# Performance work log

Measured on AMD Instinct MI355X. Metric: run time of the kernel, lower is better.

## Reference

```python
import jax, jax.numpy as jnp
import numpy as np

B, S, D, H = 4, 2048, 1024, 16
HD = D // H


def setup_inputs() -> dict:
    key = jax.random.key(0)
    ks = jax.random.split(key, 12)
    scale = 1.0 / np.sqrt(D)
    inp = {
        "query": jax.random.normal(ks[0], (B, S, D), jnp.float32),
        "key": jax.random.normal(ks[1], (B, S, D), jnp.float32),
        "value": jax.random.normal(ks[2], (B, S, D), jnp.float32),
        "mask": jax.random.randint(ks[3], (B, 1, S, S), 0, 2).astype(jnp.float32),
        "Wq": jax.random.normal(ks[4], (D, D), jnp.float32) * scale,
        "bq": jnp.zeros((D,), jnp.float32),
        "Wk": jax.random.normal(ks[5], (D, D), jnp.float32) * scale,
        "bk": jnp.zeros((D,), jnp.float32),
        "Wv": jax.random.normal(ks[6], (D, D), jnp.float32) * scale,
        "bv": jnp.zeros((D,), jnp.float32),
        "Wo": jax.random.normal(ks[7], (D, D), jnp.float32) * scale,
        "bo": jnp.zeros((D,), jnp.float32),
    }
    return inp


def reference(query, key, value, mask, Wq, bq, Wk, bk, Wv, bv, Wo, bo):
    # projections, then split heads: [B, S, D] -> [B, H, S, HD]
    def split_heads(x):
        return x.reshape(B, S, H, HD).transpose(0, 2, 1, 3)

    q = split_heads(query @ Wq + bq)
    k = split_heads(key @ Wk + bk)
    v = split_heads(value @ Wv + bv)

    # scores [B, H, Sq, Sk]
    logits = jnp.einsum("bhqd,bhkd->bhqk", q, k) / jnp.sqrt(jnp.float32(HD))
    logits = logits + mask * (-1e9)
    attn = jax.nn.softmax(logits, axis=-1)
    out = jnp.einsum("bhqk,bhkd->bhqd", attn, v)  # [B, H, Sq, HD]
    out = out.transpose(0, 2, 1, 3).reshape(B, S, D)
    return out @ Wo + bo
```

## Files before the change

kernel.cpp:

```cpp
#include <hip/hip_runtime.h>

#define DI __device__ __forceinline__

typedef __attribute__((ext_vector_type(8))) short short8v;
typedef __attribute__((ext_vector_type(4))) float f32x4;

static constexpr int B_ = 4, S_ = 2048, D_ = 1024, H_ = 16, HD_ = 64;
static constexpr int M_ = B_ * S_;

DI unsigned short f2bf(float f) {
  unsigned u = __builtin_bit_cast(unsigned, f);
  u = (u + 0x7fffu + ((u >> 16) & 1u)) >> 16;
  return (unsigned short)u;
}

DI unsigned cvt_pk_bf16(float lo, float hi) {
  unsigned r;
  asm("v_cvt_pk_bf16_f32 %0, %1, %2" : "=v"(r) : "v"(lo), "v"(hi));
  return r;
}

DI void async_copy16(const void* g, void* l) {
  __builtin_amdgcn_global_load_lds((const __attribute__((address_space(1))) void*)g,
                                   (__attribute__((address_space(3))) void*)l, 16, 0, 0);
}

__global__ __launch_bounds__(256) void cast_bf16_kernel(const float* __restrict__ in,
                                                        unsigned short* __restrict__ out,
                                                        int n4) {
  int i = blockIdx.x * blockDim.x + threadIdx.x;
  int stride = gridDim.x * blockDim.x;
  for (; i < n4; i += stride) {
    float4 v = reinterpret_cast<const float4*>(in)[i];
    ushort4 o;
    o.x = f2bf(v.x); o.y = f2bf(v.y); o.z = f2bf(v.z); o.w = f2bf(v.w);
    reinterpret_cast<ushort4*>(out)[i] = o;
  }
}

__global__ __launch_bounds__(256) void transpose_cast_kernel(const float* __restrict__ W,
                                                             unsigned short* __restrict__ Wt,
                                                             int n) {
  __shared__ float t[32][33];
  int bx = blockIdx.x * 32, by = blockIdx.y * 32;
  int x = threadIdx.x, y0 = threadIdx.y;
#pragma unroll
  for (int yy = 0; yy < 32; yy += 8)
    t[y0 + yy][x] = W[(long)(by + y0 + yy) * n + bx + x];
  __syncthreads();
#pragma unroll
  for (int yy = 0; yy < 32; yy += 8)
    Wt[(long)(bx + y0 + yy) * n + by + x] = f2bf(t[x][y0 + yy]);
}

__global__ __launch_bounds__(256) void pack_mask_kernel(const float* __restrict__ mask,
                                                        unsigned long long* __restrict__ bits,
                                                        int nwords) {
  int lane = threadIdx.x & 63;
  int wpb = blockDim.x >> 6;
  int w = blockIdx.x * wpb + (threadIdx.x >> 6);
  int stride = gridDim.x * wpb;
  for (; w < nwords; w += stride) {
    float v = mask[(long)w * 64 + lane];
    unsigned long long b = __ballot(v > 0.5f);
    if (lane == 0) {
      int bb = w >> 16, q = (w >> 5) & 2047, kt64 = w & 31;
      bits[((long)bb << 16) | (kt64 << 11) | q] = b;
    }
  }
}

template <int MODE>
__global__ __launch_bounds__(256) void gemm_bt_kernel(const unsigned short* __restrict__ A,
                                                      const unsigned short* __restrict__ Bt,
                                                      const float* __restrict__ bias,
                                                      void* __restrict__ out,
                                                      int Mdim, int Ndim, int Kdim, float scale) {
  __shared__ unsigned short As[3][128 * 32];
  __shared__ unsigned short Bs[3][128 * 32];
  const int tid = threadIdx.x;
  const int lane = tid & 63;
  const int w = tid >> 6;
  const int g = lane >> 4;
  const int l15 = lane & 15;
  const int bm = blockIdx.x * 128;
  const int bn = blockIdx.y * 128;
  const int wr = w >> 1, wc = w & 1;

  f32x4 zero = {0.f, 0.f, 0.f, 0.f};
  f32x4 acc[4][4];
#pragma unroll
  for (int i = 0; i < 4; ++i)
#pragma unroll
    for (int j = 0; j < 4; ++j) acc[i][j] = zero;

  const int srow = lane >> 2;
  const int scol = (lane & 3) * 8;

  auto stageg = [&](int k0, int bi) {
#pragma unroll
    for (int i = 0; i < 2; ++i) {
      int q = w * 2 + i;
      int row = q * 16 + srow;
      async_copy16(&A[(long)(bm + row) * Kdim + k0 + scol], &As[bi][q * 512]);
      async_copy16(&Bt[(long)(bn + row) * Kdim + k0 + scol], &Bs[bi][q * 512]);
    }
  };

  const int NT = Kdim / 32;
  stageg(0, 0);
  stageg(32, 1);
  asm volatile("s_waitcnt vmcnt(4)" ::: "memory");
  __builtin_amdgcn_sched_barrier(0);
  __builtin_amdgcn_s_barrier();
  asm volatile("" ::: "memory");

  for (int t = 0; t < NT; ++t) {
    if (t + 2 < NT) stageg((t + 2) * 32, (t + 2) % 3);

    const unsigned short* Ab = &As[t % 3][0];
    const unsigned short* Bb = &Bs[t % 3][0];
    short8v a[4], b[4];
#pragma unroll
    for (int i = 0; i < 4; ++i)
      a[i] = *reinterpret_cast<const short8v*>(&Ab[(wr * 64 + i * 16 + l15) * 32 + g * 8]);
#pragma unroll
    for (int j = 0; j < 4; ++j)
      b[j] = *reinterpret_cast<const short8v*>(&Bb[(wc * 64 + j * 16 + l15) * 32 + g * 8]);
#pragma unroll
    for (int i = 0; i < 4; ++i)
#pragma unroll
      for (int j = 0; j < 4; ++j)
        acc[i][j] = __builtin_amdgcn_mfma_f32_16x16x32_bf16(a[i], b[j], acc[i][j], 0, 0, 0);

    if (t + 2 < NT) {
      asm volatile("s_waitcnt vmcnt(4) lgkmcnt(0)" ::: "memory");
    } else {
      asm volatile("s_waitcnt vmcnt(0) lgkmcnt(0)" ::: "memory");
    }
    __builtin_amdgcn_sched_barrier(0);
    __builtin_amdgcn_s_barrier();
    asm volatile("" ::: "memory");
  }

#pragma unroll
  for (int jj = 0; jj < 4; ++jj) {
    int n = bn + wc * 64 + jj * 16 + l15;
    float bs = bias[n];
#pragma unroll
    for (int i = 0; i < 4; ++i) {
      int m0 = bm + wr * 64 + i * 16 + g * 4;
      if (MODE == 0) {
        unsigned short* o = (unsigned short*)out;
#pragma unroll
        for (int r = 0; r < 4; ++r)
          o[(long)(m0 + r) * Ndim + n] = f2bf((acc[i][jj][r] + bs) * scale);
      } else if (MODE == 1) {
        int b2 = m0 >> 11, s0 = m0 & 2047;
        int s0p = (s0 & ~31) | (((s0 >> 2) & 3) << 3) | (((s0 >> 4) & 1) << 2);
        int h2 = n >> 6, d2 = n & 63;
        unsigned short* o = (unsigned short*)out;
        ushort4 v;
        v.x = f2bf(acc[i][jj][0] + bs);
        v.y = f2bf(acc[i][jj][1] + bs);
        v.z = f2bf(acc[i][jj][2] + bs);
        v.w = f2bf(acc[i][jj][3] + bs);
        *reinterpret_cast<ushort4*>(&o[((long)((b2 * 16 + h2) * 64 + d2) << 11) + s0p]) = v;
      } else {
        float* o = (float*)out;
#pragma unroll
        for (int r = 0; r < 4; ++r)
          o[(long)(m0 + r) * Ndim + n] = acc[i][jj][r] + bs;
      }
    }
  }
}

__global__ __launch_bounds__(256, 4) void attn_kernel(const unsigned short* __restrict__ Q,
                                                      const unsigned short* __restrict__ Kb,
                                                      const unsigned short* __restrict__ Vt,
                                                      const unsigned long long* __restrict__ mbits,
                                                      unsigned short* __restrict__ attn) {
  __shared__ unsigned short Ks[2][64 * 64];
  __shared__ unsigned short Vs[2][64 * 64];
  const int lane = threadIdx.x & 63;
  const int w = threadIdx.x >> 6;
  const int g = lane >> 4;
  const int l15 = lane & 15;
  const int qt = blockIdx.x;
  const int bh = blockIdx.y;
  const int b = bh >> 4, h = bh & 15;
  const int q0 = qt * 64 + w * 16 + l15;

  const unsigned short* qp = Q + ((long)b * S_ + q0) * D_ + h * HD_ + g * 8;
  short8v qf0 = *reinterpret_cast<const short8v*>(qp);
  short8v qf1 = *reinterpret_cast<const short8v*>(qp + 32);

  const int srow = lane >> 3;
  const int schunk = ((lane & 7) ^ (lane >> 3)) * 8;
  const unsigned short* kstage = Kb + (long)b * S_ * D_ + h * HD_;
  const unsigned short* vstage = Vt + (long)bh * HD_ * S_;

  f32x4 zero = {0.f, 0.f, 0.f, 0.f};
  f32x4 oacc[4] = {zero, zero, zero, zero};
  float m_run = -1e30f, l_run = 0.f;

  const unsigned long long* mbase = mbits + ((long)b << 16);
  const int swz = l15 & 7;

  auto stage = [&](int kt, int bi) {
#pragma unroll
    for (int i = 0; i < 2; ++i) {
      int blk8 = w * 2 + i;
      async_copy16(&kstage[(long)(kt + blk8 * 8 + srow) * D_ + schunk], &Ks[bi][blk8 * 512]);
      async_copy16(&vstage[(long)(blk8 * 8 + srow) * S_ + kt + schunk], &Vs[bi][blk8 * 512]);
    }
  };

  unsigned long long mw_cur = mbase[q0];
  stage(0, 0);

  int cur = 0;
  for (int t = 0; t < S_ / 64; ++t) {
    unsigned long long mw_nxt = 0;
    if (t < S_ / 64 - 1) {
      mw_nxt = mbase[((t + 1) << 11) + q0];
      stage((t + 1) * 64, cur ^ 1);
      asm volatile("s_waitcnt vmcnt(5)" ::: "memory");
    } else {
      asm volatile("s_waitcnt vmcnt(0)" ::: "memory");
    }
    __builtin_amdgcn_s_barrier();
    asm volatile("" ::: "memory");

    const unsigned short* Kbuf = &Ks[cur][0];
    const unsigned short* Vbuf = &Vs[cur][0];

    f32x4 lt[4];
    __builtin_amdgcn_s_setprio(1);
#pragma unroll
    for (int g2 = 0; g2 < 4; ++g2) {
      const unsigned short* kr = &Kbuf[(g2 * 16 + l15) * 64];
      short8v kf0 = *reinterpret_cast<const short8v*>(&kr[(g ^ swz) * 8]);
      short8v kf1 = *reinterpret_cast<const short8v*>(&kr[((g + 4) ^ swz) * 8]);
      f32x4 c = zero;
      c = __builtin_amdgcn_mfma_f32_16x16x32_bf16(kf0, qf0, c, 0, 0, 0);
      c = __builtin_amdgcn_mfma_f32_16x16x32_bf16(kf1, qf1, c, 0, 0, 0);
      lt[g2] = c;
    }
    __builtin_amdgcn_s_setprio(0);

    float tmax = -1e30f;
#pragma unroll
    for (int g2 = 0; g2 < 4; ++g2)
#pragma unroll
      for (int r = 0; r < 4; ++r) {
        int krel = g2 * 16 + g * 4 + r;
        float v = ((mw_cur >> krel) & 1ull) ? -1e30f : lt[g2][r];
        lt[g2][r] = v;
        tmax = fmaxf(tmax, v);
      }
    tmax = fmaxf(tmax, __shfl_xor(tmax, 16));
    tmax = fmaxf(tmax, __shfl_xor(tmax, 32));
    float m_new = fmaxf(m_run, tmax);
    float alpha = __builtin_amdgcn_exp2f(m_run - m_new);
    float p[4][4];
    float tsum = 0.f;
#pragma unroll
    for (int g2 = 0; g2 < 4; ++g2)
#pragma unroll
      for (int r = 0; r < 4; ++r) {
        p[g2][r] = __builtin_amdgcn_exp2f(lt[g2][r] - m_new);
        tsum += p[g2][r];
      }
    tsum += __shfl_xor(tsum, 16);
    tsum += __shfl_xor(tsum, 32);
    l_run = l_run * alpha + tsum;
    m_run = m_new;
#pragma unroll
    for (int d = 0; d < 4; ++d) oacc[d] *= alpha;
    short8v pfr[2];
#pragma unroll
    for (int s = 0; s < 2; ++s) {
      union { unsigned u[4]; short8v v; } pu;
      pu.u[0] = cvt_pk_bf16(p[2 * s][0], p[2 * s][1]);
      pu.u[1] = cvt_pk_bf16(p[2 * s][2], p[2 * s][3]);
      pu.u[2] = cvt_pk_bf16(p[2 * s + 1][0], p[2 * s + 1][1]);
      pu.u[3] = cvt_pk_bf16(p[2 * s + 1][2], p[2 * s + 1][3]);
      pfr[s] = pu.v;
    }

    __builtin_amdgcn_s_setprio(1);
#pragma unroll
    for (int d0 = 0; d0 < 4; ++d0) {
      const unsigned short* vr = &Vbuf[(d0 * 16 + l15) * 64];
#pragma unroll
      for (int s = 0; s < 2; ++s) {
        short8v vf = *reinterpret_cast<const short8v*>(&vr[((s * 4 + g) ^ swz) * 8]);
        oacc[d0] = __builtin_amdgcn_mfma_f32_16x16x32_bf16(vf, pfr[s], oacc[d0], 0, 0, 0);
      }
    }
    __builtin_amdgcn_s_setprio(0);

    asm volatile("" ::: "memory");
    __builtin_amdgcn_s_barrier();
    asm volatile("" ::: "memory");
    mw_cur = mw_nxt;
    cur ^= 1;
  }

  float inv = 1.f / l_run;
#pragma unroll
  for (int d0 = 0; d0 < 4; ++d0) {
    ushort4 o;
    o.x = f2bf(oacc[d0][0] * inv);
    o.y = f2bf(oacc[d0][1] * inv);
    o.z = f2bf(oacc[d0][2] * inv);
    o.w = f2bf(oacc[d0][3] * inv);
    *reinterpret_cast<ushort4*>(&attn[((long)b * S_ + q0) * D_ + h * HD_ + d0 * 16 + g * 4]) = o;
  }
}

extern "C" void kernel_launch(void* const* d_in, const int* in_sizes, int n_in,
                              void* d_out, int out_size, void* d_ws, size_t ws_size,
                              hipStream_t stream) {
  const float* query = (const float*)d_in[0];
  const float* key   = (const float*)d_in[1];
  const float* value = (const float*)d_in[2];
  const float* mask  = (const float*)d_in[3];
  const float* Wq = (const float*)d_in[4];
  const float* bq = (const float*)d_in[5];
  const float* Wk = (const float*)d_in[6];
  const float* bk = (const float*)d_in[7];
  const float* Wv = (const float*)d_in[8];
  const float* bv = (const float*)d_in[9];
  const float* Wo = (const float*)d_in[10];
  const float* bo = (const float*)d_in[11];

  char* ws = (char*)d_ws;
  unsigned short* XQ  = (unsigned short*)(ws);
  unsigned short* XK  = (unsigned short*)(ws + (16ull << 20));
  unsigned short* XV  = (unsigned short*)(ws + (32ull << 20));
  unsigned short* WQT = (unsigned short*)(ws + (48ull << 20));
  unsigned short* WKT = (unsigned short*)(ws + (50ull << 20));
  unsigned short* WVT = (unsigned short*)(ws + (52ull << 20));
  unsigned short* WOT = (unsigned short*)(ws + (54ull << 20));
  unsigned short* QB  = (unsigned short*)(ws + (56ull << 20));
  unsigned short* KB  = (unsigned short*)(ws + (72ull << 20));
  unsigned short* VT  = (unsigned short*)(ws + (88ull << 20));
  unsigned long long* MBITS = (unsigned long long*)(ws + (16ull << 20));
  unsigned short* ATTN = XQ;

  const int n4 = M_ * D_ / 4;
  cast_bf16_kernel<<<2048, 256, 0, stream>>>(query, XQ, n4);
  cast_bf16_kernel<<<2048, 256, 0, stream>>>(key,   XK, n4);
  cast_bf16_kernel<<<2048, 256, 0, stream>>>(value, XV, n4);

  dim3 tg(D_ / 32, D_ / 32), tb(32, 8);
  transpose_cast_kernel<<<tg, tb, 0, stream>>>(Wq, WQT, D_);
  transpose_cast_kernel<<<tg, tb, 0, stream>>>(Wk, WKT, D_);
  transpose_cast_kernel<<<tg, tb, 0, stream>>>(Wv, WVT, D_);
  transpose_cast_kernel<<<tg, tb, 0, stream>>>(Wo, WOT, D_);

  dim3 gg(M_ / 128, D_ / 128);
  gemm_bt_kernel<0><<<gg, 256, 0, stream>>>(XQ, WQT, bq, QB, M_, D_, D_, 0.18033688011112042f);
  gemm_bt_kernel<0><<<gg, 256, 0, stream>>>(XK, WKT, bk, KB, M_, D_, D_, 1.f);
  gemm_bt_kernel<1><<<gg, 256, 0, stream>>>(XV, WVT, bv, VT, M_, D_, D_, 1.f);

  pack_mask_kernel<<<2048, 256, 0, stream>>>(mask, MBITS, B_ * S_ * S_ / 64);

  dim3 ag(S_ / 64, B_ * H_);
  attn_kernel<<<ag, 256, 0, stream>>>(QB, KB, VT, MBITS, ATTN);

  gemm_bt_kernel<2><<<gg, 256, 0, stream>>>(ATTN, WOT, bo, d_out, M_, D_, D_, 1.f);
}
```

Before: 309.8 us.

## Double attention key tile to 128 per iteration with new V swizzle

The attention kernel now processes 128 keys per loop iteration instead of 64. This halves the number of barriers, online-softmax rescales and mask loads per key, and amortises loop overhead across more MFMA work. LDS buffers double to 64 KB and register pressure rises, so launch bounds drop from 4 to 2 waves per SIMD. This reduces occupancy and the ability to hide latency.

Result: slower. 318.4 us (+2.8%).

```diff
diff --git a/kernel.cpp b/kernel.cpp
--- a/kernel.cpp
+++ b/kernel.cpp
@@ -176,13 +176,13 @@
   }
 }
 
-__global__ __launch_bounds__(256, 4) void attn_kernel(const unsigned short* __restrict__ Q,
+__global__ __launch_bounds__(256, 2) void attn_kernel(const unsigned short* __restrict__ Q,
                                                       const unsigned short* __restrict__ Kb,
                                                       const unsigned short* __restrict__ Vt,
                                                       const unsigned long long* __restrict__ mbits,
                                                       unsigned short* __restrict__ attn) {
-  __shared__ unsigned short Ks[2][64 * 64];
-  __shared__ unsigned short Vs[2][64 * 64];
+  __shared__ unsigned short Ks[2][128 * 64];
+  __shared__ unsigned short Vs[2][64 * 128];
   const int lane = threadIdx.x & 63;
   const int w = threadIdx.x >> 6;
   const int g = lane >> 4;
@@ -196,8 +196,9 @@
   short8v qf0 = *reinterpret_cast<const short8v*>(qp);
   short8v qf1 = *reinterpret_cast<const short8v*>(qp + 32);
 
-  const int srow = lane >> 3;
-  const int schunk = ((lane & 7) ^ (lane >> 3)) * 8;
+  const int srowK = lane >> 3;
+  const int schunkK = ((lane & 7) ^ (lane >> 3)) * 8;
+  const int srowV = lane >> 4;
   const unsigned short* kstage = Kb + (long)b * S_ * D_ + h * HD_;
   const unsigned short* vstage = Vt + (long)bh * HD_ * S_;
 
@@ -206,27 +207,30 @@
   float m_run = -1e30f, l_run = 0.f;
 
   const unsigned long long* mbase = mbits + ((long)b << 16);
-  const int swz = l15 & 7;
-
-  auto stage = [&](int kt, int bi) {
-#pragma unroll
-    for (int i = 0; i < 2; ++i) {
-      int blk8 = w * 2 + i;
-      async_copy16(&kstage[(long)(kt + blk8 * 8 + srow) * D_ + schunk], &Ks[bi][blk8 * 512]);
-      async_copy16(&vstage[(long)(blk8 * 8 + srow) * S_ + kt + schunk], &Vs[bi][blk8 * 512]);
+  const int swz7 = l15 & 7;
+
+  auto stage = [&](int kt, int bufi) {
+#pragma unroll
+    for (int i = 0; i < 4; ++i) {
+      int bi = w * 4 + i;
+      async_copy16(&kstage[(long)(kt + bi * 8 + srowK) * D_ + schunkK], &Ks[bufi][bi * 512]);
+      int vchunk = ((lane & 15) ^ (((bi & 3) << 2) | srowV)) * 8;
+      async_copy16(&vstage[(long)(bi * 4 + srowV) * S_ + kt + vchunk], &Vs[bufi][bi * 512]);
     }
   };
 
-  unsigned long long mw_cur = mbase[q0];
+  unsigned long long mwa = mbase[q0];
+  unsigned long long mwb = mbase[(1 << 11) + q0];
   stage(0, 0);
 
   int cur = 0;
-  for (int t = 0; t < S_ / 64; ++t) {
-    unsigned long long mw_nxt = 0;
-    if (t < S_ / 64 - 1) {
-      mw_nxt = mbase[((t + 1) << 11) + q0];
-      stage((t + 1) * 64, cur ^ 1);
-      asm volatile("s_waitcnt vmcnt(5)" ::: "memory");
+  for (int t = 0; t < S_ / 128; ++t) {
+    unsigned long long mwa_n = 0, mwb_n = 0;
+    if (t < S_ / 128 - 1) {
+      mwa_n = mbase[((2 * t + 2) << 11) + q0];
+      mwb_n = mbase[((2 * t + 3) << 11) + q0];
+      stage((t + 1) * 128, cur ^ 1);
+      asm volatile("s_waitcnt vmcnt(10)" ::: "memory");
     } else {
       asm volatile("s_waitcnt vmcnt(0)" ::: "memory");
     }
@@ -236,13 +240,13 @@
     const unsigned short* Kbuf = &Ks[cur][0];
     const unsigned short* Vbuf = &Vs[cur][0];
 
-    f32x4 lt[4];
+    f32x4 lt[8];
     __builtin_amdgcn_s_setprio(1);
 #pragma unroll
-    for (int g2 = 0; g2 < 4; ++g2) {
+    for (int g2 = 0; g2 < 8; ++g2) {
       const unsigned short* kr = &Kbuf[(g2 * 16 + l15) * 64];
-      short8v kf0 = *reinterpret_cast<const short8v*>(&kr[(g ^ swz) * 8]);
-      short8v kf1 = *reinterpret_cast<const short8v*>(&kr[((g + 4) ^ swz) * 8]);
+      short8v kf0 = *reinterpret_cast<const short8v*>(&kr[(g ^ swz7) * 8]);
+      short8v kf1 = *reinterpret_cast<const short8v*>(&kr[((g + 4) ^ swz7) * 8]);
       f32x4 c = zero;
       c = __builtin_amdgcn_mfma_f32_16x16x32_bf16(kf0, qf0, c, 0, 0, 0);
       c = __builtin_amdgcn_mfma_f32_16x16x32_bf16(kf1, qf1, c, 0, 0, 0);
@@ -252,26 +256,27 @@
 
     float tmax = -1e30f;
 #pragma unroll
-    for (int g2 = 0; g2 < 4; ++g2)
+    for (int g2 = 0; g2 < 8; ++g2) {
+      unsigned long long mw = (g2 < 4) ? mwa : mwb;
 #pragma unroll
       for (int r = 0; r < 4; ++r) {
-        int krel = g2 * 16 + g * 4 + r;
-        float v = ((mw_cur >> krel) & 1ull) ? -1e30f : lt[g2][r];
+        int krel = (g2 & 3) * 16 + g * 4 + r;
+        float v = ((mw >> krel) & 1ull) ? -1e30f : lt[g2][r];
         lt[g2][r] = v;
         tmax = fmaxf(tmax, v);
       }
+    }
     tmax = fmaxf(tmax, __shfl_xor(tmax, 16));
     tmax = fmaxf(tmax, __shfl_xor(tmax, 32));
     float m_new = fmaxf(m_run, tmax);
     float alpha = __builtin_amdgcn_exp2f(m_run - m_new);
-    float p[4][4];
     float tsum = 0.f;
 #pragma unroll
-    for (int g2 = 0; g2 < 4; ++g2)
+    for (int g2 = 0; g2 < 8; ++g2)
 #pragma unroll
       for (int r = 0; r < 4; ++r) {
-        p[g2][r] = __builtin_amdgcn_exp2f(lt[g2][r] - m_new);
-        tsum += p[g2][r];
+        lt[g2][r] = __builtin_amdgcn_exp2f(lt[g2][r] - m_new);
+        tsum += lt[g2][r];
       }
     tsum += __shfl_xor(tsum, 16);
     tsum += __shfl_xor(tsum, 32);
@@ -279,24 +284,24 @@
     m_run = m_new;
 #pragma unroll
     for (int d = 0; d < 4; ++d) oacc[d] *= alpha;
-    short8v pfr[2];
-#pragma unroll
-    for (int s = 0; s < 2; ++s) {
+    short8v pfr[4];
+#pragma unroll
+    for (int s = 0; s < 4; ++s) {
       union { unsigned u[4]; short8v v; } pu;
-      pu.u[0] = cvt_pk_bf16(p[2 * s][0], p[2 * s][1]);
-      pu.u[1] = cvt_pk_bf16(p[2 * s][2], p[2 * s][3]);
-      pu.u[2] = cvt_pk_bf16(p[2 * s + 1][0], p[2 * s + 1][1]);
-      pu.u[3] = cvt_pk_bf16(p[2 * s + 1][2], p[2 * s + 1][3]);
+      pu.u[0] = cvt_pk_bf16(lt[2 * s][0], lt[2 * s][1]);
+      pu.u[1] = cvt_pk_bf16(lt[2 * s][2], lt[2 * s][3]);
+      pu.u[2] = cvt_pk_bf16(lt[2 * s + 1][0], lt[2 * s + 1][1]);
+      pu.u[3] = cvt_pk_bf16(lt[2 * s + 1][2], lt[2 * s + 1][3]);
       pfr[s] = pu.v;
     }
 
     __builtin_amdgcn_s_setprio(1);
 #pragma unroll
     for (int d0 = 0; d0 < 4; ++d0) {
-      const unsigned short* vr = &Vbuf[(d0 * 16 + l15) * 64];
-#pragma unroll
-      for (int s = 0; s < 2; ++s) {
-        short8v vf = *reinterpret_cast<const short8v*>(&vr[((s * 4 + g) ^ swz) * 8]);
+      const unsigned short* vr = &Vbuf[(d0 * 16 + l15) * 128];
+#pragma unroll
+      for (int s = 0; s < 4; ++s) {
+        short8v vf = *reinterpret_cast<const short8v*>(&vr[((s * 4 + g) ^ l15) * 8]);
         oacc[d0] = __builtin_amdgcn_mfma_f32_16x16x32_bf16(vf, pfr[s], oacc[d0], 0, 0, 0);
       }
     }
@@ -305,7 +310,8 @@
     asm volatile("" ::: "memory");
     __builtin_amdgcn_s_barrier();
     asm volatile("" ::: "memory");
-    mw_cur = mw_nxt;
+    mwa = mwa_n;
+    mwb = mwb_n;
     cur ^= 1;
   }
 
```
